# Performance work log

Hardware: AMD Instinct MI355X
Metric: run time of the kernel (lower is better)

The kernel has to match this reference:

```python
import jax, jax.numpy as jnp
import numpy as np

B, IN_CAPS, IN_DIM = 256, 1152, 8
NUM_CAPS, DIM_VEC = 10, 16
NUM_ROUTING = 3


def squash(v, axis=-1):
    # scale = |v|^2 / (1+|v|^2) / |v|
    s2 = jnp.sum(jnp.square(v), axis=axis, keepdims=True)
    scale = s2 / (1.0 + s2) / jnp.sqrt(s2)
    return scale * v


def setup_inputs() -> dict:
    key = jax.random.key(0)
    k1, k2 = jax.random.split(key)
    inputs = jax.random.normal(k1, (B, IN_CAPS, IN_DIM), dtype=jnp.float32)
    W = jax.random.normal(k2, (IN_CAPS, NUM_CAPS, IN_DIM, DIM_VEC), dtype=jnp.float32) * 0.05
    bias = jnp.zeros((1, IN_CAPS, NUM_CAPS), dtype=jnp.float32)
    return {"inputs": inputs, "W": W, "bias": bias}


def reference(inputs, W, bias):
    # inputs_hat[b,i,j,d] = sum_e inputs[b,i,e] * W[i,j,e,d]
    hat = jnp.einsum('bie,ijed->bijd', inputs, W)  # [B, ic, nc, dv]
    b_logits = bias  # [1, ic, nc], broadcasts to [B, ic, nc] after first update
    outputs = None
    for r in range(NUM_ROUTING):
        c = jax.nn.softmax(b_logits, axis=2)            # coupling over output caps
        s = jnp.sum(c[..., None] * hat, axis=1)         # [B, nc, dv]
        outputs = squash(s)                             # [B, nc, dv]
        if r != NUM_ROUTING - 1:
            # agreement: <hat[b,i,j,:], v[b,j,:]>
            b_logits = b_logits + jnp.einsum('bijd,bjd->bij', hat, outputs)
    return outputs  # [B, num_capsule, dim_vector]
```

## Files before the change

kernel.cpp:

```cpp
#include <hip/hip_runtime.h>
#include <hip/hip_fp16.h>


#define IC 1152
#define IE 8
#define NC 10
#define DV 16
#define NB 256
#define NW (IC * NC * IE * DV)
#define SOUT (NC * DV)
#define NWAVE 12
#define TPB (NWAVE * 64)
#define NGPW 3
#define NPAIRB ((IC / 32) * NC)

typedef _Float16 h2 __attribute__((ext_vector_type(2)));
union WChunk { int4 v; h2 p[4]; _Float16 h[8]; };
union XFrag { int4 v; h2 p[4]; };

#if defined(__has_builtin) && __has_builtin(__builtin_amdgcn_fdot2)
__device__ inline float fdot2(h2 a, h2 b, float c) {
    return __builtin_amdgcn_fdot2(a, b, c, false);
}
#else
__device__ inline float fdot2(h2 a, h2 b, float c) {
    return fmaf((float)a.x, (float)b.x, fmaf((float)a.y, (float)b.y, c));
}
#endif

__global__ void wprep_kernel(const float* __restrict__ W, int4* __restrict__ Wc) {
    const int t = blockIdx.x * blockDim.x + threadIdx.x;
    if (t >= NW / 8) return;
    const int lane = t & 63;
    const int h = lane >> 5, r = lane & 31;
    const int k = (t >> 6) & 7;
    const int r2 = t >> 9;
    const int j = r2 % NC, Gp = r2 / NC;
    const int i = Gp * 32 + r;
    const int d = h * 8 + k;
    const float* src = W + ((size_t)(i * NC + j) * IE) * DV + d;
    WChunk c;
#pragma unroll
    for (int e = 0; e < IE; ++e) c.h[e] = (_Float16)src[(size_t)e * DV];
    Wc[t] = c.v;
}

template <int RD, bool HSTORE, bool HLOAD>
__global__ __launch_bounds__(TPB) void round_caps(
    const float* __restrict__ X,
    const int4* __restrict__ Wc,
    const float* __restrict__ bias,
    int4* __restrict__ hat_ws,
    const float* __restrict__ v_in,
    float* __restrict__ v_out)
{
    __shared__ float s_part[NWAVE * SOUT];
    __shared__ __align__(16) h2 v2s[SOUT / 2];

    const int b = blockIdx.x;
    const int tid = threadIdx.x;
    const int w = tid >> 6;
    const int g = tid & 63;
    const int h = g >> 5;
    const int r = g & 31;

    float vkeep = 0.f;
    if constexpr (RD > 0) {
        if (RD == 1 && tid < SOUT) vkeep = v_in[(size_t)b * SOUT + tid];
        if (tid < SOUT / 2) {
            const float* vp = v_in + (size_t)b * SOUT + 2 * tid;
            v2s[tid] = h2{(_Float16)vp[0], (_Float16)vp[1]};
        }
    }
    for (int idx = g; idx < SOUT; idx += 64) s_part[w * SOUT + idx] = 0.f;
    if constexpr (RD > 0) __syncthreads();

#pragma unroll
    for (int gl = 0; gl < NGPW; ++gl) {
        const int Gp = NGPW * w + gl;
        const int i = Gp * 32 + r;

        h2 hat2[NC][4];
        if constexpr (HLOAD) {
            const int4* hp = hat_ws + ((size_t)b * NPAIRB + Gp * NC) * 64 + g;
#pragma unroll
            for (int j = 0; j < NC; ++j) {
                WChunk u;
                u.v = hp[j * 64];
#pragma unroll
                for (int q = 0; q < 4; ++q) hat2[j][q] = u.p[q];
            }
        } else {
            XFrag xu;
            {
                const float4* xr = (const float4*)(X + ((size_t)b * IC + i) * IE);
                const float4 x0 = xr[0], x1 = xr[1];
                xu.p[0] = h2{(_Float16)x0.x, (_Float16)x0.y};
                xu.p[1] = h2{(_Float16)x0.z, (_Float16)x0.w};
                xu.p[2] = h2{(_Float16)x1.x, (_Float16)x1.y};
                xu.p[3] = h2{(_Float16)x1.z, (_Float16)x1.w};
            }
#pragma unroll
            for (int j = 0; j < NC; ++j) {
                const int4* wp = Wc + ((size_t)(Gp * NC + j)) * 512 + g;
                WChunk wk[4];
                float hat[8];
#pragma unroll
                for (int k = 0; k < 4; ++k) wk[k].v = wp[k * 64];
#pragma unroll
                for (int k = 0; k < 4; ++k) {
                    float a = 0.f;
#pragma unroll
                    for (int q = 0; q < 4; ++q) a = fdot2(xu.p[q], wk[k].p[q], a);
                    hat[k] = a;
                }
#pragma unroll
                for (int k = 0; k < 4; ++k) wk[k].v = wp[(k + 4) * 64];
#pragma unroll
                for (int k = 0; k < 4; ++k) {
                    float a = 0.f;
#pragma unroll
                    for (int q = 0; q < 4; ++q) a = fdot2(xu.p[q], wk[k].p[q], a);
                    hat[k + 4] = a;
                }
#pragma unroll
                for (int q = 0; q < 4; ++q)
                    hat2[j][q] = h2{(_Float16)hat[2 * q], (_Float16)hat[2 * q + 1]};
                if constexpr (HSTORE) {
                    WChunk u;
#pragma unroll
                    for (int q = 0; q < 4; ++q) u.p[q] = hat2[j][q];
                    hat_ws[((size_t)b * NPAIRB + Gp * NC + j) * 64 + g] = u.v;
                }
            }
        }

        float c[NC];
        {
            float Z = 0.f;
#pragma unroll
            for (int j = 0; j < NC; ++j) {
                float lt = bias[i * NC + j];
                if constexpr (RD > 0) {
                    XFrag vv;
                    vv.v = *(const int4*)(v2s + (j * 8 + h * 4));
                    float ah = 0.f;
#pragma unroll
                    for (int q = 0; q < 4; ++q) ah = fdot2(hat2[j][q], vv.p[q], ah);
                    lt += ah + __shfl_xor(ah, 32);
                }
                const float e = __expf(lt);
                c[j] = e;
                Z += e;
            }
            const float rz = 1.f / Z;
#pragma unroll
            for (int j = 0; j < NC; ++j) c[j] *= rz;
        }

#pragma unroll
        for (int j = 0; j < NC; ++j) {
            float s8[8];
#pragma unroll
            for (int q = 0; q < 4; ++q) {
                s8[2 * q]     = c[j] * (float)hat2[j][q].x;
                s8[2 * q + 1] = c[j] * (float)hat2[j][q].y;
            }
            float t4[4];
#pragma unroll
            for (int d = 0; d < 4; ++d) {
                const bool hi = (r & 16);
                const float mine = hi ? s8[d + 4] : s8[d];
                const float send = hi ? s8[d] : s8[d + 4];
                t4[d] = mine + __shfl_xor(send, 16);
            }
            float t2[2];
#pragma unroll
            for (int d = 0; d < 2; ++d) {
                const bool hi = (r & 8);
                const float mine = hi ? t4[d + 2] : t4[d];
                const float send = hi ? t4[d] : t4[d + 2];
                t2[d] = mine + __shfl_xor(send, 8);
            }
            float t1;
            {
                const bool hi = (r & 4);
                const float mine = hi ? t2[1] : t2[0];
                const float send = hi ? t2[0] : t2[1];
                t1 = mine + __shfl_xor(send, 4);
            }
            t1 += __shfl_xor(t1, 2);
            t1 += __shfl_xor(t1, 1);
            if ((r & 3) == 0) {
                const int dl = (r >> 2) & 7;
                s_part[w * SOUT + j * DV + h * 8 + dl] += t1;
            }
        }
    }
    __syncthreads();

    if (tid < SOUT) {
        float sv = 0.f;
#pragma unroll
        for (int ww = 0; ww < NWAVE; ++ww) sv += s_part[ww * SOUT + tid];
        float s2 = sv * sv;
#pragma unroll
        for (int mk = 8; mk >= 1; mk >>= 1) s2 += __shfl_xor(s2, mk, 16);
        const float scale = sqrtf(s2) / (1.f + s2);
        float vv = scale * sv;
        if constexpr (RD == 1) vv += vkeep;
        v_out[(size_t)b * SOUT + tid] = vv;
    }
}

extern "C" void kernel_launch(void* const* d_in, const int* in_sizes, int n_in,
                              void* d_out, int out_size, void* d_ws, size_t ws_size,
                              hipStream_t stream) {
    const float* X = (const float*)d_in[0];
    const float* W = (const float*)d_in[1];
    const float* bias = (const float*)d_in[2];
    float* out = (float*)d_out;

    int4* Wc = (int4*)d_ws;
    float* v1 = (float*)(Wc + NW / 8);
    float* vsum = v1 + (size_t)NB * SOUT;
    int4* hat_ws = (int4*)(vsum + (size_t)NB * SOUT);
    const size_t need = (size_t)(NW / 8) * 16 + 2ull * NB * SOUT * 4 +
                        (size_t)NB * NPAIRB * 64 * 16;

    wprep_kernel<<<dim3(720), dim3(256), 0, stream>>>(W, Wc);

    dim3 grid(NB);
    if (ws_size >= need) {
        round_caps<0, true, false><<<grid, TPB, 0, stream>>>(X, Wc, bias, hat_ws, nullptr, v1);
        round_caps<1, false, true><<<grid, TPB, 0, stream>>>(X, Wc, bias, hat_ws, v1, vsum);
        round_caps<2, false, true><<<grid, TPB, 0, stream>>>(X, Wc, bias, hat_ws, vsum, out);
    } else {
        round_caps<0, false, false><<<grid, TPB, 0, stream>>>(X, Wc, bias, nullptr, nullptr, v1);
        round_caps<1, false, false><<<grid, TPB, 0, stream>>>(X, Wc, bias, nullptr, v1, vsum);
        round_caps<2, false, false><<<grid, TPB, 0, stream>>>(X, Wc, bias, nullptr, vsum, out);
    }
}
```

Baseline: 147.7 us.

## Fuse three routing rounds into one kernel, recomputing hat per round

Replaces the three per-round launches with one kernel per batch row that loops over the routing rounds. The running sum of squashed outputs is kept in shared memory, so no intermediate v buffers go through global memory. The stored hat workspace is dropped and hat is recomputed from W and X in every round. This saves two launches and the hat write/read traffic, but triples the W reads and dot-product work.

Result: slower. 309.2 us (+109.4%).

```diff
diff --git a/kernel.cpp b/kernel.cpp
--- a/kernel.cpp
+++ b/kernel.cpp
@@ -12,7 +12,6 @@
 #define NWAVE 12
 #define TPB (NWAVE * 64)
 #define NGPW 3
-#define NPAIRB ((IC / 32) * NC)
 
 typedef _Float16 h2 __attribute__((ext_vector_type(2)));
 union WChunk { int4 v; h2 p[4]; _Float16 h[8]; };
@@ -45,16 +44,14 @@
     Wc[t] = c.v;
 }
 
-template <int RD, bool HSTORE, bool HLOAD>
-__global__ __launch_bounds__(TPB) void round_caps(
+__global__ __launch_bounds__(TPB) void caps_kernel(
     const float* __restrict__ X,
     const int4* __restrict__ Wc,
     const float* __restrict__ bias,
-    int4* __restrict__ hat_ws,
-    const float* __restrict__ v_in,
-    float* __restrict__ v_out)
+    float* __restrict__ out)
 {
     __shared__ float s_part[NWAVE * SOUT];
+    __shared__ float vc[SOUT];
     __shared__ __align__(16) h2 v2s[SOUT / 2];
 
     const int b = blockIdx.x;
@@ -64,33 +61,14 @@
     const int h = g >> 5;
     const int r = g & 31;
 
-    float vkeep = 0.f;
-    if constexpr (RD > 0) {
-        if (RD == 1 && tid < SOUT) vkeep = v_in[(size_t)b * SOUT + tid];
-        if (tid < SOUT / 2) {
-            const float* vp = v_in + (size_t)b * SOUT + 2 * tid;
-            v2s[tid] = h2{(_Float16)vp[0], (_Float16)vp[1]};
-        }
-    }
     for (int idx = g; idx < SOUT; idx += 64) s_part[w * SOUT + idx] = 0.f;
-    if constexpr (RD > 0) __syncthreads();
-
-#pragma unroll
-    for (int gl = 0; gl < NGPW; ++gl) {
-        const int Gp = NGPW * w + gl;
-        const int i = Gp * 32 + r;
-
-        h2 hat2[NC][4];
-        if constexpr (HLOAD) {
-            const int4* hp = hat_ws + ((size_t)b * NPAIRB + Gp * NC) * 64 + g;
-#pragma unroll
-            for (int j = 0; j < NC; ++j) {
-                WChunk u;
-                u.v = hp[j * 64];
-#pragma unroll
-                for (int q = 0; q < 4; ++q) hat2[j][q] = u.p[q];
-            }
-        } else {
+
+    for (int rd = 0; rd < 3; ++rd) {
+#pragma unroll
+        for (int gl = 0; gl < NGPW; ++gl) {
+            const int Gp = NGPW * w + gl;
+            const int i = Gp * 32 + r;
+
             XFrag xu;
             {
                 const float4* xr = (const float4*)(X + ((size_t)b * IC + i) * IE);
@@ -100,6 +78,8 @@
                 xu.p[2] = h2{(_Float16)x1.x, (_Float16)x1.y};
                 xu.p[3] = h2{(_Float16)x1.z, (_Float16)x1.w};
             }
+
+            h2 hat2[NC][4];
 #pragma unroll
             for (int j = 0; j < NC; ++j) {
                 const int4* wp = Wc + ((size_t)(Gp * NC + j)) * 512 + g;
@@ -126,90 +106,95 @@
 #pragma unroll
                 for (int q = 0; q < 4; ++q)
                     hat2[j][q] = h2{(_Float16)hat[2 * q], (_Float16)hat[2 * q + 1]};
-                if constexpr (HSTORE) {
-                    WChunk u;
-#pragma unroll
-                    for (int q = 0; q < 4; ++q) u.p[q] = hat2[j][q];
-                    hat_ws[((size_t)b * NPAIRB + Gp * NC + j) * 64 + g] = u.v;
+            }
+
+            float c[NC];
+            {
+                float Z = 0.f;
+#pragma unroll
+                for (int j = 0; j < NC; ++j) {
+                    float lt = bias[i * NC + j];
+                    if (rd > 0) {
+                        XFrag vv;
+                        vv.v = *(const int4*)(v2s + (j * 8 + h * 4));
+                        float ah = 0.f;
+#pragma unroll
+                        for (int q = 0; q < 4; ++q) ah = fdot2(hat2[j][q], vv.p[q], ah);
+                        lt += ah + __shfl_xor(ah, 32);
+                    }
+                    const float e = __expf(lt);
+                    c[j] = e;
+                    Z += e;
+                }
+                const float rz = 1.f / Z;
+#pragma unroll
+                for (int j = 0; j < NC; ++j) c[j] *= rz;
+            }
+
+#pragma unroll
+            for (int j = 0; j < NC; ++j) {
+                float s8[8];
+#pragma unroll
+                for (int q = 0; q < 4; ++q) {
+                    s8[2 * q]     = c[j] * (float)hat2[j][q].x;
+                    s8[2 * q + 1] = c[j] * (float)hat2[j][q].y;
+                }
+                float t4[4];
+#pragma unroll
+                for (int d = 0; d < 4; ++d) {
+                    const bool hi = (r & 16);
+                    const float mine = hi ? s8[d + 4] : s8[d];
+                    const float send = hi ? s8[d] : s8[d + 4];
+                    t4[d] = mine + __shfl_xor(send, 16);
+                }
+                float t2[2];
+#pragma unroll
+                for (int d = 0; d < 2; ++d) {
+                    const bool hi = (r & 8);
+                    const float mine = hi ? t4[d + 2] : t4[d];
+                    const float send = hi ? t4[d] : t4[d + 2];
+                    t2[d] = mine + __shfl_xor(send, 8);
+                }
+                float t1;
+                {
+                    const bool hi = (r & 4);
+                    const float mine = hi ? t2[1] : t2[0];
+                    const float send = hi ? t2[0] : t2[1];
+                    t1 = mine + __shfl_xor(send, 4);
+                }
+                t1 += __shfl_xor(t1, 2);
+                t1 += __shfl_xor(t1, 1);
+                if ((r & 3) == 0) {
+                    const int dl = (r >> 2) & 7;
+                    s_part[w * SOUT + j * DV + h * 8 + dl] += t1;
                 }
             }
         }
-
-        float c[NC];
-        {
-            float Z = 0.f;
-#pragma unroll
-            for (int j = 0; j < NC; ++j) {
-                float lt = bias[i * NC + j];
-                if constexpr (RD > 0) {
-                    XFrag vv;
-                    vv.v = *(const int4*)(v2s + (j * 8 + h * 4));
-                    float ah = 0.f;
-#pragma unroll
-                    for (int q = 0; q < 4; ++q) ah = fdot2(hat2[j][q], vv.p[q], ah);
-                    lt += ah + __shfl_xor(ah, 32);
-                }
-                const float e = __expf(lt);
-                c[j] = e;
-                Z += e;
-            }
-            const float rz = 1.f / Z;
-#pragma unroll
-            for (int j = 0; j < NC; ++j) c[j] *= rz;
+        __syncthreads();
+
+        if (tid < SOUT) {
+            float sv = 0.f;
+#pragma unroll
+            for (int ww = 0; ww < NWAVE; ++ww) sv += s_part[ww * SOUT + tid];
+            float s2 = sv * sv;
+#pragma unroll
+            for (int mk = 8; mk >= 1; mk >>= 1) s2 += __shfl_xor(s2, mk, 16);
+            const float scale = sqrtf(s2) / (1.f + s2);
+            const float vv = scale * sv;
+            if (rd == 2) {
+                out[(size_t)b * SOUT + tid] = vv;
+            } else {
+                const float vcum = (rd == 0) ? vv : (vc[tid] + vv);
+                vc[tid] = vcum;
+                const float oth = __shfl_xor(vcum, 1);
+                if (!(tid & 1)) v2s[tid >> 1] = h2{(_Float16)vcum, (_Float16)oth};
+            }
         }
-
-#pragma unroll
-        for (int j = 0; j < NC; ++j) {
-            float s8[8];
-#pragma unroll
-            for (int q = 0; q < 4; ++q) {
-                s8[2 * q]     = c[j] * (float)hat2[j][q].x;
-                s8[2 * q + 1] = c[j] * (float)hat2[j][q].y;
-            }
-            float t4[4];
-#pragma unroll
-            for (int d = 0; d < 4; ++d) {
-                const bool hi = (r & 16);
-                const float mine = hi ? s8[d + 4] : s8[d];
-                const float send = hi ? s8[d] : s8[d + 4];
-                t4[d] = mine + __shfl_xor(send, 16);
-            }
-            float t2[2];
-#pragma unroll
-            for (int d = 0; d < 2; ++d) {
-                const bool hi = (r & 8);
-                const float mine = hi ? t4[d + 2] : t4[d];
-                const float send = hi ? t4[d] : t4[d + 2];
-                t2[d] = mine + __shfl_xor(send, 8);
-            }
-            float t1;
-            {
-                const bool hi = (r & 4);
-                const float mine = hi ? t2[1] : t2[0];
-                const float send = hi ? t2[0] : t2[1];
-                t1 = mine + __shfl_xor(send, 4);
-            }
-            t1 += __shfl_xor(t1, 2);
-            t1 += __shfl_xor(t1, 1);
-            if ((r & 3) == 0) {
-                const int dl = (r >> 2) & 7;
-                s_part[w * SOUT + j * DV + h * 8 + dl] += t1;
-            }
+        __syncthreads();
+
+        if (rd < 2) {
+            for (int idx = g; idx < SOUT; idx += 64) s_part[w * SOUT + idx] = 0.f;
         }
-    }
-    __syncthreads();
-
-    if (tid < SOUT) {
-        float sv = 0.f;
-#pragma unroll
-        for (int ww = 0; ww < NWAVE; ++ww) sv += s_part[ww * SOUT + tid];
-        float s2 = sv * sv;
-#pragma unroll
-        for (int mk = 8; mk >= 1; mk >>= 1) s2 += __shfl_xor(s2, mk, 16);
-        const float scale = sqrtf(s2) / (1.f + s2);
-        float vv = scale * sv;
-        if constexpr (RD == 1) vv += vkeep;
-        v_out[(size_t)b * SOUT + tid] = vv;
     }
 }
 
@@ -222,22 +207,7 @@
     float* out = (float*)d_out;
 
     int4* Wc = (int4*)d_ws;
-    float* v1 = (float*)(Wc + NW / 8);
-    float* vsum = v1 + (size_t)NB * SOUT;
-    int4* hat_ws = (int4*)(vsum + (size_t)NB * SOUT);
-    const size_t need = (size_t)(NW / 8) * 16 + 2ull * NB * SOUT * 4 +
-                        (size_t)NB * NPAIRB * 64 * 16;
 
     wprep_kernel<<<dim3(720), dim3(256), 0, stream>>>(W, Wc);
-
-    dim3 grid(NB);
-    if (ws_size >= need) {
-        round_caps<0, true, false><<<grid, TPB, 0, stream>>>(X, Wc, bias, hat_ws, nullptr, v1);
-        round_caps<1, false, true><<<grid, TPB, 0, stream>>>(X, Wc, bias, hat_ws, v1, vsum);
-        round_caps<2, false, true><<<grid, TPB, 0, stream>>>(X, Wc, bias, hat_ws, vsum, out);
-    } else {
-        round_caps<0, false, false><<<grid, TPB, 0, stream>>>(X, Wc, bias, nullptr, nullptr, v1);
-        round_caps<1, false, false><<<grid, TPB, 0, stream>>>(X, Wc, bias, nullptr, v1, vsum);
-        round_caps<2, false, false><<<grid, TPB, 0, stream>>>(X, Wc, bias, nullptr, vsum, out);
-    }
-}
+    caps_kernel<<<dim3(NB), dim3(TPB), 0, stream>>>(X, Wc, bias, out);
+}
```
